# Kernel optimization log

Hardware: AMD Instinct MI355X
Metric: run time of the kernel (lower is better)

## Reference

```python
import jax, jax.numpy as jnp
import numpy as np

NUM_CLASSES = 256


def setup_inputs() -> dict:
    key = jax.random.key(0)
    k1, k2, k3, k4 = jax.random.split(key, 4)
    N, D = 16384, 512
    src_feat = jax.random.normal(k1, (N, D), dtype=jnp.float32)
    trg_feat = jax.random.normal(k2, (N, D), dtype=jnp.float32)
    src_label = jax.random.randint(k3, (N,), 0, NUM_CLASSES, dtype=jnp.int32)
    trg_label = jax.random.randint(k4, (N,), 0, NUM_CLASSES, dtype=jnp.int32)
    return {"src_feat": src_feat, "trg_feat": trg_feat,
            "src_label": src_label, "trg_label": trg_label}


def _kl_mean(x_log, t_log):
    # F.kl_div(input=x_log, target=t_log) with target treated as log-probs
    # (intended semantics): mean over all elements of p_t * (log p_t - x_log)
    return jnp.mean(jnp.exp(t_log) * (t_log - x_log))


def reference(src_feat, trg_feat, src_label, trg_label):
    C = NUM_CLASSES
    ones_s = jnp.ones(src_label.shape, src_feat.dtype)
    ones_t = jnp.ones(trg_label.shape, trg_feat.dtype)
    cnt_s = jax.ops.segment_sum(ones_s, src_label, num_segments=C)  # [C]
    cnt_t = jax.ops.segment_sum(ones_t, trg_label, num_segments=C)
    sum_s = jax.ops.segment_sum(src_feat, src_label, num_segments=C)  # [C,D]
    sum_t = jax.ops.segment_sum(trg_feat, trg_label, num_segments=C)
    u_s = sum_s / cnt_s[:, None]
    u_t = sum_t / cnt_t[:, None]
    u_st = (sum_s + sum_t) / (cnt_s + cnt_t)[:, None]

    feats = jnp.concatenate((src_feat, trg_feat), axis=0)  # [Ns+Nt, D]
    ls = jax.nn.log_softmax(feats @ u_s.T, axis=-1)   # [Ns+Nt, C]
    lt = jax.nn.log_softmax(feats @ u_t.T, axis=-1)
    lst = jax.nn.log_softmax(feats @ u_st.T, axis=-1)

    loss_st = 0.5 * (_kl_mean(ls, lt) + _kl_mean(lt, ls))
    loss_sst = 0.5 * (_kl_mean(ls, lst) + _kl_mean(lst, ls))
    loss_tst = 0.5 * (_kl_mean(lt, lst) + _kl_mean(lst, lt))
    return (loss_st + loss_sst + loss_tst) / 3.0
```

## Files before the change

kernel.cpp:

```cpp
#include <hip/hip_runtime.h>
#include <hip/hip_bf16.h>

#define NN 16384
#define DD 512
#define CC 256
#define CAP 192

typedef short bf16x8 __attribute__((ext_vector_type(8)));
typedef float f32x4 __attribute__((ext_vector_type(4)));
typedef float f32x16 __attribute__((ext_vector_type(16)));

__device__ __forceinline__ short f2bf(float x) {
  __hip_bfloat16 h = __float2bfloat16(x);
  return __builtin_bit_cast(short, h);
}

__global__ void k_bucket(const int* __restrict__ lab_s, const int* __restrict__ lab_t,
                         int* __restrict__ cur, int* __restrict__ idx) {
  const int i = blockIdx.x * 256 + threadIdx.x;
  const int t = i >> 14, r = i & 16383;
  const int c = (t ? lab_t : lab_s)[r];
  const int tc = t * 256 + c;
  const int pos = atomicAdd(&cur[tc], 1);
  if (pos < CAP) idx[tc * CAP + pos] = r;
}

__global__ void k_gather(const float* __restrict__ src, const float* __restrict__ trg,
                         const int* __restrict__ cur, const int* __restrict__ idx,
                         float* __restrict__ sum_s, float* __restrict__ sum_t,
                         float* __restrict__ cnt_s, float* __restrict__ cnt_t) {
  const int tc = blockIdx.x;
  const int t = tc >> 8, c = tc & 255;
  const float* feat = t ? trg : src;
  float* sum = t ? sum_t : sum_s;
  float* cnt = t ? cnt_t : cnt_s;
  const int tid = threadIdx.x;
  const int q = tid & 127, h = tid >> 7;
  const int count = min(cur[tc], CAP);

  __shared__ int lidx[CAP];
  __shared__ f32x4 sh[128];
  if (tid < count) lidx[tid] = idx[tc * CAP + tid];
  __syncthreads();

  f32x4 a = (f32x4){0.f, 0.f, 0.f, 0.f};
  f32x4 b = (f32x4){0.f, 0.f, 0.f, 0.f};
  int r = h;
  for (; r + 2 < count; r += 4) {
    a += *reinterpret_cast<const f32x4*>(feat + (size_t)lidx[r] * DD + q * 4);
    b += *reinterpret_cast<const f32x4*>(feat + (size_t)lidx[r + 2] * DD + q * 4);
  }
  if (r < count)
    a += *reinterpret_cast<const f32x4*>(feat + (size_t)lidx[r] * DD + q * 4);
  a += b;
  if (h == 1) sh[q] = a;
  __syncthreads();
  if (h == 0) {
    a += sh[q];
    *reinterpret_cast<f32x4*>(sum + c * DD + q * 4) = a;
    if (tid == 0) cnt[c] = (float)count;
  }
}

__global__ void k_u(const float* __restrict__ sum_s, const float* __restrict__ sum_t,
                    const float* __restrict__ cnt_s, const float* __restrict__ cnt_t,
                    unsigned short* __restrict__ Upk, float* __restrict__ wcol) {
  const int c = blockIdx.x, tid = threadIdx.x;
  const float cs = cnt_s[c], ct = cnt_t[c];
  const float rs = 1.f / cs, rt = 1.f / ct;
  const int t32 = c >> 5, col31 = c & 31;
#pragma unroll
  for (int kk = 0; kk < 2; ++kk) {
    const int k = tid + kk * 256;
    const float ss = sum_s[c * DD + k], st = sum_t[c * DD + k];
    const int kc = k >> 5, ks = (k >> 4) & 1, hi = (k >> 3) & 1, j = k & 7;
    const int e = kc * 8192 + t32 * 1024 + ks * 512 + (col31 + 32 * hi) * 8 + j;
    Upk[0 * 131072 + e] = (unsigned short)f2bf(ss * rs);
    Upk[1 * 131072 + e] = (unsigned short)f2bf(st * rt);
  }
  if (tid == 0) wcol[c] = cs / (cs + ct);
}

__global__ __launch_bounds__(1024, 4) void k_main(
    const float* __restrict__ src, const float* __restrict__ trg,
    const unsigned short* __restrict__ Upk, const float* __restrict__ wcol,
    float* __restrict__ out) {
  __shared__ short SMEM[81920];
  short* const Bs0 = &SMEM[0];
  short* const As0 = &SMEM[65536];

  const int tid = threadIdx.x;
  const int w = tid >> 6, lane = tid & 63;
  const int hi = lane >> 5, l31 = lane & 31;
  const int wr = w >> 2, cw = w & 3;
  const int row0 = blockIdx.x * 128;
  const float* feat = (row0 < NN) ? src + (size_t)row0 * DD
                                  : trg + (size_t)(row0 - NN) * DD;

  const int ar = tid >> 3, aq = tid & 7;
  const float* aglob = feat + (size_t)ar * DD + aq * 8;
  const int kcs = aq >> 2, q4 = aq & 3;
  const int awoff = kcs * 4096 + (ar >> 5) * 1024 + (q4 >> 1) * 512 +
                    ((ar & 31) + 32 * (q4 & 1)) * 8;

  f32x16 acc[2][2];
#pragma unroll
  for (int m = 0; m < 2; ++m)
#pragma unroll
    for (int ct = 0; ct < 2; ++ct)
#pragma unroll
      for (int r = 0; r < 16; ++r) acc[m][ct][r] = 0.f;

  auto stageB = [&](int kc8, int buf) {
#pragma unroll
    for (int s = 0; s < 4; ++s) {
      const int u = s * 16 + w;
      const int uk = u >> 5, mat = (u >> 4) & 1, t16 = u & 15;
      const unsigned short* g = Upk + (size_t)mat * 131072 +
                                (kc8 * 2 + uk) * 8192 + t16 * 512 + lane * 8;
      __builtin_amdgcn_global_load_lds(
          (const __attribute__((address_space(1))) unsigned int*)g,
          (__attribute__((address_space(3))) unsigned int*)&Bs0[buf * 32768 + u * 512],
          16, 0, 0);
    }
  };
  auto writeA = [&](const float4& v0, const float4& v1, int buf) {
    bf16x8 b;
    b[0] = f2bf(v0.x); b[1] = f2bf(v0.y); b[2] = f2bf(v0.z); b[3] = f2bf(v0.w);
    b[4] = f2bf(v1.x); b[5] = f2bf(v1.y); b[6] = f2bf(v1.z); b[7] = f2bf(v1.w);
    *reinterpret_cast<bf16x8*>(&As0[buf * 8192 + awoff]) = b;
  };
  auto compute = [&](int buf) {
#pragma unroll
    for (int kk = 0; kk < 2; ++kk) {
      const bf16x8 a0 = *reinterpret_cast<const bf16x8*>(
          &As0[buf * 8192 + kk * 4096 + wr * 1024 + 0 * 512 + lane * 8]);
      const bf16x8 a1 = *reinterpret_cast<const bf16x8*>(
          &As0[buf * 8192 + kk * 4096 + wr * 1024 + 1 * 512 + lane * 8]);
#pragma unroll
      for (int m = 0; m < 2; ++m)
#pragma unroll
        for (int ct = 0; ct < 2; ++ct) {
          const int t32 = cw * 2 + ct;
          const bf16x8 b0 = *reinterpret_cast<const bf16x8*>(
              &Bs0[buf * 32768 + kk * 16384 + (m * 16 + t32 * 2 + 0) * 512 + lane * 8]);
          const bf16x8 b1 = *reinterpret_cast<const bf16x8*>(
              &Bs0[buf * 32768 + kk * 16384 + (m * 16 + t32 * 2 + 1) * 512 + lane * 8]);
          acc[m][ct] = __builtin_amdgcn_mfma_f32_32x32x16_bf16(a0, b0, acc[m][ct], 0, 0, 0);
          acc[m][ct] = __builtin_amdgcn_mfma_f32_32x32x16_bf16(a1, b1, acc[m][ct], 0, 0, 0);
        }
    }
  };

  float4 af0 = *reinterpret_cast<const float4*>(aglob);
  float4 af1 = *reinterpret_cast<const float4*>(aglob + 4);
  asm volatile("" ::: "memory");
  stageB(0, 0);
  writeA(af0, af1, 0);

#pragma unroll 1
  for (int kc8 = 0; kc8 < 8; ++kc8) {
    asm volatile("s_waitcnt vmcnt(0) lgkmcnt(0)" ::: "memory");
    if (kc8 < 7) {
      af0 = *reinterpret_cast<const float4*>(aglob + (kc8 + 1) * 64);
      af1 = *reinterpret_cast<const float4*>(aglob + (kc8 + 1) * 64 + 4);
    }
    __builtin_amdgcn_s_barrier();
    if (kc8 < 7) stageB(kc8 + 1, (kc8 + 1) & 1);
    compute(kc8 & 1);
    if (kc8 < 7) writeA(af0, af1, (kc8 + 1) & 1);
  }

  const float wv0 = wcol[(cw * 2 + 0) * 32 + l31];
  const float wv1 = wcol[(cw * 2 + 1) * 32 + l31];
  f32x16 ca0, ca1;
#pragma unroll
  for (int r = 0; r < 16; ++r) {
    ca0[r] = wv0 * acc[0][0][r] + (1.f - wv0) * acc[1][0][r];
    ca1[r] = wv1 * acc[0][1][r] + (1.f - wv1) * acc[1][1][r];
  }

  __syncthreads();
  float* T = (float*)&SMEM[0];
  float* sLseF = T + 16640;
  float* bredF = T + 17024;
  const int erow = tid >> 4, ecc = tid & 15;

  auto lsePass = [&](const f32x16& vA, const f32x16& vB, int m) {
#pragma unroll
    for (int h = 0; h < 2; ++h) {
      if ((wr >> 1) == h) {
        const int lr0 = (wr & 1) * 32;
#pragma unroll
        for (int r = 0; r < 16; ++r) {
          const int lr = lr0 + (r & 3) + 8 * (r >> 2) + 4 * hi;
          T[lr * 260 + (cw * 2 + 0) * 32 + l31] = vA[r];
          T[lr * 260 + (cw * 2 + 1) * 32 + l31] = vB[r];
        }
      }
      __syncthreads();
      float s = 0.f;
      const float* tb = &T[erow * 260 + ecc * 16];
#pragma unroll
      for (int j = 0; j < 4; ++j) {
        const f32x4 x = *reinterpret_cast<const f32x4*>(tb + j * 4);
        s += __expf(x[0]) + __expf(x[1]) + __expf(x[2]) + __expf(x[3]);
      }
      s += __shfl_xor(s, 1); s += __shfl_xor(s, 2);
      s += __shfl_xor(s, 4); s += __shfl_xor(s, 8);
      if (ecc == 0) sLseF[m * 128 + h * 64 + erow] = __logf(s);
      __syncthreads();
    }
  };
  lsePass(acc[0][0], acc[0][1], 0);
  lsePass(acc[1][0], acc[1][1], 1);
  lsePass(ca0, ca1, 2);

  float ks = 0.f;
#pragma unroll
  for (int r = 0; r < 16; ++r) {
    const int row = wr * 32 + (r & 3) + 8 * (r >> 2) + 4 * hi;
    {
      const float a = acc[0][0][r] - sLseF[row];
      const float b = acc[1][0][r] - sLseF[128 + row];
      const float c = ca0[r] - sLseF[256 + row];
      ks += __expf(a) * (2.f * a - b - c) + __expf(b) * (2.f * b - a - c) +
            __expf(c) * (2.f * c - a - b);
    }
    {
      const float a = acc[0][1][r] - sLseF[row];
      const float b = acc[1][1][r] - sLseF[128 + row];
      const float c = ca1[r] - sLseF[256 + row];
      ks += __expf(a) * (2.f * a - b - c) + __expf(b) * (2.f * b - a - c) +
            __expf(c) * (2.f * c - a - b);
    }
  }
#pragma unroll
  for (int off = 1; off < 64; off <<= 1)
    ks += __shfl_xor(ks, off);
  if (lane == 0) bredF[w] = ks;
  __syncthreads();
  if (tid == 0) {
    float s = 0.f;
#pragma unroll
    for (int i = 0; i < 16; ++i) s += bredF[i];
    atomicAdd(out, s * (1.f / 50331648.f));
  }
}

extern "C" void kernel_launch(void* const* d_in, const int* in_sizes, int n_in,
                              void* d_out, int out_size, void* d_ws, size_t ws_size,
                              hipStream_t stream) {
  const float* src = (const float*)d_in[0];
  const float* trg = (const float*)d_in[1];
  const int* lab_s = (const int*)d_in[2];
  const int* lab_t = (const int*)d_in[3];
  float* out = (float*)d_out;

  char* p = (char*)d_ws;
  float* sum_s = (float*)p;                  p += 524288;
  float* sum_t = (float*)p;                  p += 524288;
  float* cnt_s = (float*)p;                  p += 1024;
  float* cnt_t = (float*)p;                  p += 1024;
  int* cur = (int*)p;                        p += 2048;
  int* idx = (int*)p;                        p += 512 * CAP * 4;
  unsigned short* Upk = (unsigned short*)p;  p += 2 * 131072 * 2;
  float* wcol = (float*)p;                   p += 1024;

  hipMemsetAsync(cur, 0, 2048, stream);
  hipMemsetAsync(out, 0, (size_t)out_size * sizeof(float), stream);
  k_bucket<<<128, 256, 0, stream>>>(lab_s, lab_t, cur, idx);
  k_gather<<<512, 256, 0, stream>>>(src, trg, cur, idx, sum_s, sum_t, cnt_s, cnt_t);
  k_u<<<CC, 256, 0, stream>>>(sum_s, sum_t, cnt_s, cnt_t, Upk, wcol);
  k_main<<<256, 1024, 0, stream>>>(src, trg, Upk, wcol, out);
}
```

Before: 69.89 us.

## Fuse mean normalization into gather, drop k_u and memset, remap main-kernel warps

The gather kernel now divides the class sums by their count and writes bf16 means directly in the packed MFMA layout. This removes the k_u launch and the fp32 sum round trip through memory. The output zeroing moves into k_bucket, which removes one memset, and the mixing weight is computed from the counts inside k_main. The main kernel's warp mapping changes so each warp covers two row tiles by one column tile, reusing each B fragment across two rows instead of each A fragment across two column tiles.

```diff
diff --git a/kernel.cpp b/kernel.cpp
--- a/kernel.cpp
+++ b/kernel.cpp
@@ -7,6 +7,7 @@
 #define CAP 192
 
 typedef short bf16x8 __attribute__((ext_vector_type(8)));
+typedef short bf16x4 __attribute__((ext_vector_type(4)));
 typedef float f32x4 __attribute__((ext_vector_type(4)));
 typedef float f32x16 __attribute__((ext_vector_type(16)));
 
@@ -16,8 +17,10 @@
 }
 
 __global__ void k_bucket(const int* __restrict__ lab_s, const int* __restrict__ lab_t,
-                         int* __restrict__ cur, int* __restrict__ idx) {
+                         int* __restrict__ cur, int* __restrict__ idx,
+                         float* __restrict__ out) {
   const int i = blockIdx.x * 256 + threadIdx.x;
+  if (i == 0) *out = 0.f;
   const int t = i >> 14, r = i & 16383;
   const int c = (t ? lab_t : lab_s)[r];
   const int tc = t * 256 + c;
@@ -27,13 +30,11 @@
 
 __global__ void k_gather(const float* __restrict__ src, const float* __restrict__ trg,
                          const int* __restrict__ cur, const int* __restrict__ idx,
-                         float* __restrict__ sum_s, float* __restrict__ sum_t,
+                         unsigned short* __restrict__ Upk,
                          float* __restrict__ cnt_s, float* __restrict__ cnt_t) {
   const int tc = blockIdx.x;
   const int t = tc >> 8, c = tc & 255;
   const float* feat = t ? trg : src;
-  float* sum = t ? sum_t : sum_s;
-  float* cnt = t ? cnt_t : cnt_s;
   const int tid = threadIdx.x;
   const int q = tid & 127, h = tid >> 7;
   const int count = min(cur[tc], CAP);
@@ -57,34 +58,23 @@
   __syncthreads();
   if (h == 0) {
     a += sh[q];
-    *reinterpret_cast<f32x4*>(sum + c * DD + q * 4) = a;
-    if (tid == 0) cnt[c] = (float)count;
-  }
-}
-
-__global__ void k_u(const float* __restrict__ sum_s, const float* __restrict__ sum_t,
-                    const float* __restrict__ cnt_s, const float* __restrict__ cnt_t,
-                    unsigned short* __restrict__ Upk, float* __restrict__ wcol) {
-  const int c = blockIdx.x, tid = threadIdx.x;
-  const float cs = cnt_s[c], ct = cnt_t[c];
-  const float rs = 1.f / cs, rt = 1.f / ct;
-  const int t32 = c >> 5, col31 = c & 31;
-#pragma unroll
-  for (int kk = 0; kk < 2; ++kk) {
-    const int k = tid + kk * 256;
-    const float ss = sum_s[c * DD + k], st = sum_t[c * DD + k];
-    const int kc = k >> 5, ks = (k >> 4) & 1, hi = (k >> 3) & 1, j = k & 7;
-    const int e = kc * 8192 + t32 * 1024 + ks * 512 + (col31 + 32 * hi) * 8 + j;
-    Upk[0 * 131072 + e] = (unsigned short)f2bf(ss * rs);
-    Upk[1 * 131072 + e] = (unsigned short)f2bf(st * rt);
-  }
-  if (tid == 0) wcol[c] = cs / (cs + ct);
+    const float inv = 1.f / (float)count;
+    const int t32 = c >> 5, col31 = c & 31;
+    const int k = q * 4;
+    const int kc = k >> 5, ks = (k >> 4) & 1, khi = (k >> 3) & 1, j = k & 7;
+    const int e = kc * 8192 + t32 * 1024 + ks * 512 + (col31 + 32 * khi) * 8 + j;
+    bf16x4 bb;
+    bb[0] = f2bf(a[0] * inv); bb[1] = f2bf(a[1] * inv);
+    bb[2] = f2bf(a[2] * inv); bb[3] = f2bf(a[3] * inv);
+    *reinterpret_cast<bf16x4*>(&Upk[(size_t)t * 131072 + e]) = bb;
+    if (tid == 0) (t ? cnt_t : cnt_s)[c] = (float)count;
+  }
 }
 
 __global__ __launch_bounds__(1024, 4) void k_main(
     const float* __restrict__ src, const float* __restrict__ trg,
-    const unsigned short* __restrict__ Upk, const float* __restrict__ wcol,
-    float* __restrict__ out) {
+    const unsigned short* __restrict__ Upk, const float* __restrict__ cnt_s,
+    const float* __restrict__ cnt_t, float* __restrict__ out) {
   __shared__ short SMEM[81920];
   short* const Bs0 = &SMEM[0];
   short* const As0 = &SMEM[65536];
@@ -92,7 +82,7 @@
   const int tid = threadIdx.x;
   const int w = tid >> 6, lane = tid & 63;
   const int hi = lane >> 5, l31 = lane & 31;
-  const int wr = w >> 2, cw = w & 3;
+  const int rp = w >> 3, t32w = w & 7;
   const int row0 = blockIdx.x * 128;
   const float* feat = (row0 < NN) ? src + (size_t)row0 * DD
                                   : trg + (size_t)(row0 - NN) * DD;
@@ -107,9 +97,9 @@
 #pragma unroll
   for (int m = 0; m < 2; ++m)
 #pragma unroll
-    for (int ct = 0; ct < 2; ++ct)
-#pragma unroll
-      for (int r = 0; r < 16; ++r) acc[m][ct][r] = 0.f;
+    for (int rt = 0; rt < 2; ++rt)
+#pragma unroll
+      for (int r = 0; r < 16; ++r) acc[m][rt][r] = 0.f;
 
   auto stageB = [&](int kc8, int buf) {
 #pragma unroll
@@ -133,22 +123,25 @@
   auto compute = [&](int buf) {
 #pragma unroll
     for (int kk = 0; kk < 2; ++kk) {
-      const bf16x8 a0 = *reinterpret_cast<const bf16x8*>(
-          &As0[buf * 8192 + kk * 4096 + wr * 1024 + 0 * 512 + lane * 8]);
-      const bf16x8 a1 = *reinterpret_cast<const bf16x8*>(
-          &As0[buf * 8192 + kk * 4096 + wr * 1024 + 1 * 512 + lane * 8]);
-#pragma unroll
-      for (int m = 0; m < 2; ++m)
-#pragma unroll
-        for (int ct = 0; ct < 2; ++ct) {
-          const int t32 = cw * 2 + ct;
-          const bf16x8 b0 = *reinterpret_cast<const bf16x8*>(
-              &Bs0[buf * 32768 + kk * 16384 + (m * 16 + t32 * 2 + 0) * 512 + lane * 8]);
-          const bf16x8 b1 = *reinterpret_cast<const bf16x8*>(
-              &Bs0[buf * 32768 + kk * 16384 + (m * 16 + t32 * 2 + 1) * 512 + lane * 8]);
-          acc[m][ct] = __builtin_amdgcn_mfma_f32_32x32x16_bf16(a0, b0, acc[m][ct], 0, 0, 0);
-          acc[m][ct] = __builtin_amdgcn_mfma_f32_32x32x16_bf16(a1, b1, acc[m][ct], 0, 0, 0);
+      bf16x8 a[2][2];
+#pragma unroll
+      for (int rt = 0; rt < 2; ++rt)
+#pragma unroll
+        for (int ks = 0; ks < 2; ++ks)
+          a[rt][ks] = *reinterpret_cast<const bf16x8*>(
+              &As0[buf * 8192 + kk * 4096 + (rp * 2 + rt) * 1024 + ks * 512 + lane * 8]);
+#pragma unroll
+      for (int m = 0; m < 2; ++m) {
+        const bf16x8 b0 = *reinterpret_cast<const bf16x8*>(
+            &Bs0[buf * 32768 + kk * 16384 + (m * 16 + t32w * 2 + 0) * 512 + lane * 8]);
+        const bf16x8 b1 = *reinterpret_cast<const bf16x8*>(
+            &Bs0[buf * 32768 + kk * 16384 + (m * 16 + t32w * 2 + 1) * 512 + lane * 8]);
+#pragma unroll
+        for (int rt = 0; rt < 2; ++rt) {
+          acc[m][rt] = __builtin_amdgcn_mfma_f32_32x32x16_bf16(a[rt][0], b0, acc[m][rt], 0, 0, 0);
+          acc[m][rt] = __builtin_amdgcn_mfma_f32_32x32x16_bf16(a[rt][1], b1, acc[m][rt], 0, 0, 0);
         }
+      }
     }
   };
 
@@ -171,14 +164,15 @@
     if (kc8 < 7) writeA(af0, af1, (kc8 + 1) & 1);
   }
 
-  const float wv0 = wcol[(cw * 2 + 0) * 32 + l31];
-  const float wv1 = wcol[(cw * 2 + 1) * 32 + l31];
-  f32x16 ca0, ca1;
-#pragma unroll
-  for (int r = 0; r < 16; ++r) {
-    ca0[r] = wv0 * acc[0][0][r] + (1.f - wv0) * acc[1][0][r];
-    ca1[r] = wv1 * acc[0][1][r] + (1.f - wv1) * acc[1][1][r];
-  }
+  const float csv = cnt_s[t32w * 32 + l31];
+  const float ctv = cnt_t[t32w * 32 + l31];
+  const float wv = csv / (csv + ctv);
+  f32x16 ca[2];
+#pragma unroll
+  for (int rt = 0; rt < 2; ++rt)
+#pragma unroll
+    for (int r = 0; r < 16; ++r)
+      ca[rt][r] = wv * acc[0][rt][r] + (1.f - wv) * acc[1][rt][r];
 
   __syncthreads();
   float* T = (float*)&SMEM[0];
@@ -186,16 +180,15 @@
   float* bredF = T + 17024;
   const int erow = tid >> 4, ecc = tid & 15;
 
-  auto lsePass = [&](const f32x16& vA, const f32x16& vB, int m) {
+  auto lsePass = [&](const f32x16& v0, const f32x16& v1, int m) {
 #pragma unroll
     for (int h = 0; h < 2; ++h) {
-      if ((wr >> 1) == h) {
-        const int lr0 = (wr & 1) * 32;
+      if (rp == h) {
 #pragma unroll
         for (int r = 0; r < 16; ++r) {
-          const int lr = lr0 + (r & 3) + 8 * (r >> 2) + 4 * hi;
-          T[lr * 260 + (cw * 2 + 0) * 32 + l31] = vA[r];
-          T[lr * 260 + (cw * 2 + 1) * 32 + l31] = vB[r];
+          const int lrb = (r & 3) + 8 * (r >> 2) + 4 * hi;
+          T[(0 * 32 + lrb) * 260 + t32w * 32 + l31] = v0[r];
+          T[(1 * 32 + lrb) * 260 + t32w * 32 + l31] = v1[r];
         }
       }
       __syncthreads();
@@ -214,27 +207,20 @@
   };
   lsePass(acc[0][0], acc[0][1], 0);
   lsePass(acc[1][0], acc[1][1], 1);
-  lsePass(ca0, ca1, 2);
+  lsePass(ca[0], ca[1], 2);
 
   float ks = 0.f;
 #pragma unroll
-  for (int r = 0; r < 16; ++r) {
-    const int row = wr * 32 + (r & 3) + 8 * (r >> 2) + 4 * hi;
-    {
-      const float a = acc[0][0][r] - sLseF[row];
-      const float b = acc[1][0][r] - sLseF[128 + row];
-      const float c = ca0[r] - sLseF[256 + row];
+  for (int rt = 0; rt < 2; ++rt)
+#pragma unroll
+    for (int r = 0; r < 16; ++r) {
+      const int row = rp * 64 + rt * 32 + (r & 3) + 8 * (r >> 2) + 4 * hi;
+      const float a = acc[0][rt][r] - sLseF[row];
+      const float b = acc[1][rt][r] - sLseF[128 + row];
+      const float c = ca[rt][r] - sLseF[256 + row];
       ks += __expf(a) * (2.f * a - b - c) + __expf(b) * (2.f * b - a - c) +
             __expf(c) * (2.f * c - a - b);
     }
-    {
-      const float a = acc[0][1][r] - sLseF[row];
-      const float b = acc[1][1][r] - sLseF[128 + row];
-      const float c = ca1[r] - sLseF[256 + row];
-      ks += __expf(a) * (2.f * a - b - c) + __expf(b) * (2.f * b - a - c) +
-            __expf(c) * (2.f * c - a - b);
-    }
-  }
 #pragma unroll
   for (int off = 1; off < 64; off <<= 1)
     ks += __shfl_xor(ks, off);
@@ -258,19 +244,14 @@
   float* out = (float*)d_out;
 
   char* p = (char*)d_ws;
-  float* sum_s = (float*)p;                  p += 524288;
-  float* sum_t = (float*)p;                  p += 524288;
   float* cnt_s = (float*)p;                  p += 1024;
   float* cnt_t = (float*)p;                  p += 1024;
   int* cur = (int*)p;                        p += 2048;
   int* idx = (int*)p;                        p += 512 * CAP * 4;
   unsigned short* Upk = (unsigned short*)p;  p += 2 * 131072 * 2;
-  float* wcol = (float*)p;                   p += 1024;
 
   hipMemsetAsync(cur, 0, 2048, stream);
-  hipMemsetAsync(out, 0, (size_t)out_size * sizeof(float), stream);
-  k_bucket<<<128, 256, 0, stream>>>(lab_s, lab_t, cur, idx);
-  k_gather<<<512, 256, 0, stream>>>(src, trg, cur, idx, sum_s, sum_t, cnt_s, cnt_t);
-  k_u<<<CC, 256, 0, stream>>>(sum_s, sum_t, cnt_s, cnt_t, Upk, wcol);
-  k_main<<<256, 1024, 0, stream>>>(src, trg, Upk, wcol, out);
-}
+  k_bucket<<<128, 256, 0, stream>>>(lab_s, lab_t, cur, idx, out);
+  k_gather<<<512, 256, 0, stream>>>(src, trg, cur, idx, Upk, cnt_s, cnt_t);
+  k_main<<<256, 1024, 0, stream>>>(src, trg, Upk, cnt_s, cnt_t, out);
+}
```

Measured after the change: 66.10 us. -5.4%, faster.
